# Optimization experiments

Hardware: AMD Instinct MI355X
Metric: run time of the kernel (lower is better)

The kernel has to match this reference:

```python
import jax, jax.numpy as jnp
import numpy as np

B, T, D, H = 4, 4096, 1024, 16
CAP = 0.5


def setup_inputs() -> dict:
    key = jax.random.key(0)
    ks = jax.random.split(key, 8)
    s = 0.02
    n = lambda k, shape: jax.random.normal(k, shape, dtype=jnp.float32) * s
    return {
        "x": jax.random.normal(ks[0], (B, T, D), dtype=jnp.float32),
        "w_router": n(ks[1], (D,)),
        "in_proj_w": n(ks[2], (3 * D, D)),
        "in_proj_b": jnp.zeros((3 * D,), jnp.float32),
        "out_proj_w": n(ks[3], (D, D)),
        "out_proj_b": jnp.zeros((D,), jnp.float32),
        "w1": n(ks[4], (4 * D, D)),
        "b1": jnp.zeros((4 * D,), jnp.float32),
        "w2": n(ks[5], (D, 4 * D)),
        "b2": jnp.zeros((D,), jnp.float32),
        "ln1_g": jnp.ones((D,), jnp.float32),
        "ln1_b": jnp.zeros((D,), jnp.float32),
        "ln2_g": jnp.ones((D,), jnp.float32),
        "ln2_b": jnp.zeros((D,), jnp.float32),
    }


def _ln(x, g, b, eps=1e-5):
    mu = jnp.mean(x, -1, keepdims=True)
    var = jnp.var(x, -1, keepdims=True)  # population variance, matches torch LayerNorm
    return (x - mu) * jax.lax.rsqrt(var + eps) * g + b


def reference(x, w_router, in_proj_w, in_proj_b, out_proj_w, out_proj_b,
              w1, b1, w2, b2, ln1_g, ln1_b, ln2_g, ln2_b):
    Bx, Tx, Dx = x.shape
    k = max(1, int(Tx * CAP))  # tokens routed through the block, same k for every batch row
    logits = x @ w_router  # (B,T) scalar router scores
    aux = jnp.mean(logits ** 2) * 0.01
    # top-k selection; sort indices ascending = boolean-mask gather order in torch
    idx = jnp.sort(jax.lax.top_k(logits, k)[1], axis=-1)  # (B,k)
    xs = jnp.take_along_axis(x, idx[:, :, None], axis=1)  # (B,k,D)

    h = _ln(xs, ln1_g, ln1_b)
    qkv = h @ in_proj_w.T + in_proj_b  # (B,k,3D)
    q, kk, v = jnp.split(qkv, 3, axis=-1)
    dh = Dx // H
    heads = lambda t: t.reshape(Bx, k, H, dh).transpose(0, 2, 1, 3)  # (B,H,k,dh)
    q, kk, v = heads(q), heads(kk), heads(v)
    scores = jnp.einsum('bhqd,bhkd->bhqk', q, kk) / jnp.sqrt(jnp.float32(dh))
    attn = jax.nn.softmax(scores, axis=-1)
    o = jnp.einsum('bhqk,bhkd->bhqd', attn, v).transpose(0, 2, 1, 3).reshape(Bx, k, Dx)
    o = o @ out_proj_w.T + out_proj_b
    xs = xs + o
    h2 = _ln(xs, ln2_g, ln2_b)
    ff = jax.nn.gelu(h2 @ w1.T + b1, approximate=False) @ w2.T + b2
    xs = xs + ff
    # scatter processed tokens back; unselected tokens pass through unchanged
    out = x.at[jnp.arange(Bx)[:, None], idx].set(xs)
    return out, aux
```

## Files before the change

### kernel.cpp

```cpp
#include <hip/hip_runtime.h>

#define B_    4
#define T_    4096
#define D_    1024
#define H_    16
#define DH_   64
#define KTOK  2048
#define MROWS (B_*KTOK)

typedef unsigned short u16;
typedef __attribute__((ext_vector_type(8))) short short8;
typedef __attribute__((ext_vector_type(4))) float f32x4;
typedef __attribute__((ext_vector_type(4))) unsigned int u32x4;
typedef __attribute__((ext_vector_type(2))) unsigned int u32x2;
typedef __attribute__((ext_vector_type(4))) unsigned short u16x4;

static __device__ __forceinline__ u16 f2bf(float f) {
  union { float f; unsigned int u; } a; a.f = f;
  unsigned int u = a.u;
  unsigned int r = (u + 0x7FFFu + ((u >> 16) & 1u)) >> 16;
  return (u16)r;
}

#if defined(__has_builtin)
#if __has_builtin(__builtin_amdgcn_exp2f)
#define EXP2F(x) __builtin_amdgcn_exp2f(x)
#endif
#endif
#ifndef EXP2F
#define EXP2F(x) exp2f(x)
#endif

static __device__ __forceinline__ unsigned int pkbf_t(float a, float b) {
  unsigned int ua = __builtin_bit_cast(unsigned int, a);
  unsigned int ub = __builtin_bit_cast(unsigned int, b);
  return __builtin_amdgcn_perm(ub, ua, 0x07060302u);
}

static __device__ __forceinline__ void gld_lds16(const u16* g, u16* l) {
  __builtin_amdgcn_global_load_lds((__attribute__((address_space(1))) void*)g,
                                   (__attribute__((address_space(3))) void*)l, 16, 0, 0);
}

__global__ void __launch_bounds__(256) router_kernel(const float* __restrict__ x,
    const float* __restrict__ wr, float* __restrict__ logits, float* __restrict__ auxacc)
{
  int tid = threadIdx.x; int lane = tid & 63, wave = tid >> 6;
  int row = blockIdx.x * 4 + wave;
  const float* xr = x + (size_t)row * D_;
  float dot = 0.f;
#pragma unroll
  for (int j = 0; j < 4; j++) {
    int c = j * 256 + lane * 4;
    f32x4 xv = *(const f32x4*)(xr + c);
    f32x4 wv = *(const f32x4*)(wr + c);
    dot += xv[0]*wv[0] + xv[1]*wv[1] + xv[2]*wv[2] + xv[3]*wv[3];
  }
#pragma unroll
  for (int d = 1; d < 64; d <<= 1) dot += __shfl_xor(dot, d);
  __shared__ float red[4];
  if (lane == 0) { logits[row] = dot; red[wave] = dot; }
  __syncthreads();
  if (tid == 0) {
    float a = red[0]*red[0] + red[1]*red[1] + red[2]*red[2] + red[3]*red[3];
    atomicAdd(auxacc, a);
  }
}

__global__ void __launch_bounds__(256) rank_kernel(const float* __restrict__ logits,
    int* __restrict__ mask, int* __restrict__ idx,
    const float* __restrict__ acc, float* __restrict__ auxout)
{
  __shared__ float ll[T_];
  int b = blockIdx.y;
  int tid = threadIdx.x;
  if (b == 0 && blockIdx.x == 0 && tid == 0)
    auxout[0] = acc[0] * (0.01f / (float)(B_ * T_));
  const float* lg = logits + (size_t)b * T_;
  for (int j = tid; j < T_; j += 256) ll[j] = lg[j];
  __syncthreads();
  int t = blockIdx.x * 256 + tid;
  float my = ll[t];
  int rank = 0;
  for (int j = 0; j < T_; j += 4) {
    f32x4 lj = *(const f32x4*)&ll[j];
    rank += (lj[0] > my) || (lj[0] == my && (j+0) < t);
    rank += (lj[1] > my) || (lj[1] == my && (j+1) < t);
    rank += (lj[2] > my) || (lj[2] == my && (j+2) < t);
    rank += (lj[3] > my) || (lj[3] == my && (j+3) < t);
  }
  int sel = (rank < KTOK) ? 1 : 0;
  mask[(size_t)b * T_ + t] = sel;
  if (sel) idx[b * KTOK + rank] = t;
}

__global__ void __launch_bounds__(256) passthru_kernel(const float* __restrict__ x,
    const int* __restrict__ mask, float* __restrict__ out)
{
  int row = blockIdx.x;
  if (mask[row]) return;
  const float* s = x + (size_t)row * D_;
  float* d = out + (size_t)row * D_;
  *(f32x4*)(d + threadIdx.x * 4) = *(const f32x4*)(s + threadIdx.x * 4);
}

template<bool GATHER>
__global__ void __launch_bounds__(256) ln_kernel(const float* __restrict__ src,
    const int* __restrict__ idx, const float* __restrict__ g, const float* __restrict__ bb,
    float* __restrict__ xs_out, u16* __restrict__ hout)
{
  int row = blockIdx.x;
  int tid = threadIdx.x;
  const float* srow;
  if (GATHER) {
    int b = row >> 11, i = row & (KTOK - 1);
    int t = idx[b * KTOK + i];
    srow = src + ((size_t)b * T_ + t) * D_;
  } else {
    srow = src + (size_t)row * D_;
  }
  f32x4 v = *(const f32x4*)(srow + tid * 4);
  float s  = v[0] + v[1] + v[2] + v[3];
  float sq = v[0]*v[0] + v[1]*v[1] + v[2]*v[2] + v[3]*v[3];
#pragma unroll
  for (int d = 1; d < 64; d <<= 1) { s += __shfl_xor(s, d); sq += __shfl_xor(sq, d); }
  __shared__ float rs[4], rq[4];
  int lane = tid & 63, wave = tid >> 6;
  if (lane == 0) { rs[wave] = s; rq[wave] = sq; }
  __syncthreads();
  s  = rs[0] + rs[1] + rs[2] + rs[3];
  sq = rq[0] + rq[1] + rq[2] + rq[3];
  float mean = s * (1.0f / D_);
  float var  = sq * (1.0f / D_) - mean * mean;
  float rstd = rsqrtf(var + 1e-5f);
  f32x4 gg = *(const f32x4*)(g + tid * 4);
  f32x4 bv = *(const f32x4*)(bb + tid * 4);
  if (GATHER) *(f32x4*)(xs_out + (size_t)row * D_ + tid * 4) = v;
  u16x4 o;
#pragma unroll
  for (int j = 0; j < 4; j++) o[j] = f2bf((v[j] - mean) * rstd * gg[j] + bv[j]);
  *(u16x4*)(hout + (size_t)row * D_ + tid * 4) = o;
}

__global__ void __launch_bounds__(256) f2bf_all(const float* __restrict__ s0, const float* __restrict__ s1,
    const float* __restrict__ s2, const float* __restrict__ s3,
    u16* __restrict__ d0, u16* __restrict__ d1, u16* __restrict__ d2, u16* __restrict__ d3)
{
  const size_t c0 = (size_t)3 * D_ * D_, c1 = (size_t)4 * D_ * D_, c2 = (size_t)8 * D_ * D_;
  size_t e = (size_t)blockIdx.x * 1024 + (size_t)threadIdx.x * 4;
  const float* s; u16* d; size_t off;
  if (e < c0)      { s = s0; d = d0; off = e; }
  else if (e < c1) { s = s1; d = d1; off = e - c0; }
  else if (e < c2) { s = s2; d = d2; off = e - c1; }
  else             { s = s3; d = d3; off = e - c2; }
  f32x4 v = *(const f32x4*)(s + off);
  u16x4 o; o[0]=f2bf(v[0]); o[1]=f2bf(v[1]); o[2]=f2bf(v[2]); o[3]=f2bf(v[3]);
  *(u16x4*)(d + off) = o;
}

template<int EPI>
__global__ void __launch_bounds__(256, 2) gemm_bt(
    const u16* __restrict__ A, const u16* __restrict__ W,
    const float* __restrict__ bias, float* __restrict__ xs,
    u16* __restrict__ Cb, float* __restrict__ outf,
    const int* __restrict__ idx, u16* __restrict__ vtb, int M, int N, int K)
{
  __shared__ u16 As[2][128 * 32];
  __shared__ u16 Ws[2][128 * 32];
  const int tid = threadIdx.x;
  const int lane = tid & 63, wave = tid >> 6;
  const int wm = wave >> 1, wn = wave & 1;
  const int m16 = lane & 15, quad = lane >> 4;

  const int gx = gridDim.x;
  const int id = blockIdx.y * gx + blockIdx.x;
  const int cpx = (gx * (int)gridDim.y) >> 3;
  const int tl = (id & 7) * cpx + (id >> 3);
  const int bx = tl % gx, by = tl / gx;

  const size_t arow0 = (size_t)by * 128;
  const size_t wrow0 = (size_t)bx * 128;
  const int r4 = lane >> 2, c8 = (lane & 3) * 8;

  const u16* ag0 = A + (arow0 + wave * 16 + r4) * (size_t)K + c8;
  const u16* ag1 = ag0 + (size_t)64 * K;
  const u16* wg0 = W + (wrow0 + wave * 16 + r4) * (size_t)K + c8;
  const u16* wg1 = wg0 + (size_t)64 * K;

  auto stage = [&](int k0, int s) {
    gld_lds16(ag0 + k0, &As[s][0] + (wave * 16) * 32);
    gld_lds16(ag1 + k0, &As[s][0] + (64 + wave * 16) * 32);
    gld_lds16(wg0 + k0, &Ws[s][0] + (wave * 16) * 32);
    gld_lds16(wg1 + k0, &Ws[s][0] + (64 + wave * 16) * 32);
  };

  f32x4 acc[4][4];
#pragma unroll
  for (int i = 0; i < 4; i++)
#pragma unroll
    for (int j = 0; j < 4; j++) acc[i][j] = (f32x4)0.0f;

  stage(0, 0);
  __syncthreads();
  int cur = 0;
  for (int k0 = 0; k0 < K; k0 += 32) {
    if (k0 + 32 < K) stage(k0 + 32, cur ^ 1);
    short8 af[4], wf[4];
#pragma unroll
    for (int mt = 0; mt < 4; mt++)
      af[mt] = *(const short8*)(&As[cur][0] + (wm * 64 + mt * 16 + m16) * 32 + quad * 8);
#pragma unroll
    for (int nt = 0; nt < 4; nt++)
      wf[nt] = *(const short8*)(&Ws[cur][0] + (wn * 64 + nt * 16 + m16) * 32 + quad * 8);
#pragma unroll
    for (int mt = 0; mt < 4; mt++)
#pragma unroll
      for (int nt = 0; nt < 4; nt++)
        acc[mt][nt] = __builtin_amdgcn_mfma_f32_16x16x32_bf16(af[mt], wf[nt], acc[mt][nt], 0, 0, 0);
    __syncthreads();
    cur ^= 1;
  }

#pragma unroll
  for (int mt = 0; mt < 4; mt++) {
#pragma unroll
    for (int nt = 0; nt < 4; nt++) {
      f32x4 a = acc[mt][nt];
      size_t col = wrow0 + wn * 64 + nt * 16 + m16;
      float bvv = bias[col];
      size_t rowb = arow0 + wm * 64 + mt * 16 + quad * 4;
      if (EPI == 0) {
        if ((int)col < 2 * D_) {
          float sc = ((int)col < D_) ? 0.18033688f : 1.0f;
#pragma unroll
          for (int r = 0; r < 4; r++)
            Cb[(rowb + r) * (size_t)N + col] = f2bf((a[r] + bvv) * sc);
        } else {
          int hdh = (int)col - 2 * D_;
          int bb  = (int)(rowb >> 11);
          int tok = (int)(rowb & (KTOK - 1));
          u16x4 o;
#pragma unroll
          for (int r = 0; r < 4; r++) o[r] = f2bf(a[r] + bvv);
          *(u16x4*)&vtb[(((size_t)(bb * H_) + (hdh >> 6)) * 64 + (hdh & 63)) * KTOK + tok] = o;
        }
      } else if (EPI == 1) {
#pragma unroll
        for (int r = 0; r < 4; r++) {
          size_t o = (rowb + r) * (size_t)N + col;
          xs[o] = xs[o] + (a[r] + bvv);
        }
      } else if (EPI == 2) {
#pragma unroll
        for (int r = 0; r < 4; r++) {
          float v = a[r] + bvv;
          float gv = 0.5f * v * (1.0f + erff(v * 0.70710678118654752f));
          Cb[(rowb + r) * (size_t)N + col] = f2bf(gv);
        }
      } else {
#pragma unroll
        for (int r = 0; r < 4; r++) {
          size_t row = rowb + r;
          int b = (int)(row >> 11);
          int i = (int)(row & (KTOK - 1));
          int t = idx[b * KTOK + i];
          float vv = xs[row * (size_t)D_ + col] + (a[r] + bvv);
          outf[((size_t)b * T_ + t) * D_ + col] = vv;
        }
      }
    }
  }
}

#define PSTR 72
__global__ void __launch_bounds__(256, 3) attn_kernel(const u16* __restrict__ qkv,
                                                      const u16* __restrict__ vtb,
                                                      u16* __restrict__ obuf)
{
  __shared__ u16 Ks[2][64 * 64];
  __shared__ u16 Vs[2][64 * 64];
  __shared__ u16 Ps[4][16 * PSTR];

  const int tid = threadIdx.x;
  const int lane = tid & 63, wave = tid >> 6;
  const int m16 = lane & 15, quad = lane >> 4;
  const int bh = blockIdx.x;
  const int b = bh >> 4, h = bh & 15;
  const int q0 = blockIdx.y * 128 + wave * 32;

  const u16* base = qkv + ((size_t)b * KTOK) * (3 * D_) + h * DH_;
  const u16* vb   = vtb + (size_t)bh * 64 * KTOK;

  short8 qf[2][2];
#pragma unroll
  for (int qh = 0; qh < 2; qh++) {
    const u16* qrow = base + (size_t)(q0 + qh * 16 + m16) * (3 * D_);
    qf[qh][0] = *(const short8*)(qrow + quad * 8);
    qf[qh][1] = *(const short8*)(qrow + 32 + quad * 8);
  }

  f32x4 oacc[2][4];
#pragma unroll
  for (int qh = 0; qh < 2; qh++)
#pragma unroll
    for (int nt = 0; nt < 4; nt++) oacc[qh][nt] = (f32x4)0.0f;
  f32x4 lsum[2] = {(f32x4)0.0f, (f32x4)0.0f};

  auto stage_tile = [&](const u16* g0, size_t rstride, u16* lds) {
#pragma unroll
    for (int c = 0; c < 2; c++) {
      int g = c * 256 + tid;
      int key = g >> 3;
      int cc = (g ^ key) & 7;
      gld_lds16(g0 + (size_t)key * rstride + cc * 8,
                lds + (size_t)(c * 256 + (tid & ~63)) * 8);
    }
  };

  stage_tile(base + D_, 3 * D_, &Ks[0][0]);
  stage_tile(vb, KTOK, &Vs[0][0]);
  __syncthreads();

  int buf = 0;
  for (int tk = 0; tk < KTOK; tk += 64) {
    if (tk + 64 < KTOK) {
      stage_tile(base + (size_t)(tk + 64) * (3 * D_) + D_, 3 * D_, &Ks[buf ^ 1][0]);
      stage_tile(vb + (tk + 64), KTOK, &Vs[buf ^ 1][0]);
    }
    const u16* Kb = &Ks[buf][0];
    const u16* Vb = &Vs[buf][0];

    f32x4 sacc[2][4];
#pragma unroll
    for (int qh = 0; qh < 2; qh++)
#pragma unroll
      for (int nt = 0; nt < 4; nt++) sacc[qh][nt] = (f32x4)0.0f;
    __builtin_amdgcn_s_setprio(1);
#pragma unroll
    for (int nt = 0; nt < 4; nt++) {
      int row = nt * 16 + m16;
      int sw = row & 7;
      short8 kf0 = *(const short8*)&Kb[row * 64 + ((quad ^ sw) * 8)];
      short8 kf1 = *(const short8*)&Kb[row * 64 + (((4 + quad) ^ sw) * 8)];
#pragma unroll
      for (int qh = 0; qh < 2; qh++) {
        sacc[qh][nt] = __builtin_amdgcn_mfma_f32_16x16x32_bf16(kf0, qf[qh][0], sacc[qh][nt], 0, 0, 0);
        sacc[qh][nt] = __builtin_amdgcn_mfma_f32_16x16x32_bf16(kf1, qf[qh][1], sacc[qh][nt], 0, 0, 0);
      }
    }
    __builtin_amdgcn_s_setprio(0);

    short8 vf[4][2];
#pragma unroll
    for (int nt = 0; nt < 4; nt++) {
      int row = nt * 16 + m16;
      int sw = row & 7;
      vf[nt][0] = *(const short8*)&Vb[row * 64 + ((quad ^ sw) * 8)];
      vf[nt][1] = *(const short8*)&Vb[row * 64 + (((4 + quad) ^ sw) * 8)];
    }

#pragma unroll
    for (int qh = 0; qh < 2; qh++) {
#pragma unroll
      for (int nt = 0; nt < 4; nt++) {
        f32x4 p;
#pragma unroll
        for (int r = 0; r < 4; r++) p[r] = EXP2F(sacc[qh][nt][r]);
        lsum[qh] += p;
        u32x2 w2; w2[0] = pkbf_t(p[0], p[1]); w2[1] = pkbf_t(p[2], p[3]);
        *(u32x2*)&Ps[wave][m16 * PSTR + nt * 16 + quad * 4] = w2;
      }
      short8 pa0 = *(const short8*)&Ps[wave][m16 * PSTR + quad * 8];
      short8 pa1 = *(const short8*)&Ps[wave][m16 * PSTR + 32 + quad * 8];
      __builtin_amdgcn_s_setprio(1);
#pragma unroll
      for (int nt = 0; nt < 4; nt++) {
        oacc[qh][nt] = __builtin_amdgcn_mfma_f32_16x16x32_bf16(pa0, vf[nt][0], oacc[qh][nt], 0, 0, 0);
        oacc[qh][nt] = __builtin_amdgcn_mfma_f32_16x16x32_bf16(pa1, vf[nt][1], oacc[qh][nt], 0, 0, 0);
      }
      __builtin_amdgcn_s_setprio(0);
    }

    __syncthreads();
    buf ^= 1;
  }

  float rl[2][4];
#pragma unroll
  for (int qh = 0; qh < 2; qh++) {
    float l = (lsum[qh][0] + lsum[qh][1]) + (lsum[qh][2] + lsum[qh][3]);
    l += __shfl_xor(l, 16);
    l += __shfl_xor(l, 32);
#pragma unroll
    for (int r = 0; r < 4; r++) {
      float lr = __shfl(l, (lane & 48) | (quad * 4 + r));
      rl[qh][r] = 1.0f / lr;
    }
  }

#pragma unroll
  for (int qh = 0; qh < 2; qh++)
#pragma unroll
    for (int nt = 0; nt < 4; nt++)
#pragma unroll
      for (int r = 0; r < 4; r++) {
        int qq = q0 + qh * 16 + quad * 4 + r;
        float v = oacc[qh][nt][r] * rl[qh][r];
        obuf[((size_t)b * KTOK + qq) * D_ + h * DH_ + nt * 16 + m16] = f2bf(v);
      }
}

extern "C" void kernel_launch(void* const* d_in, const int* in_sizes, int n_in,
                              void* d_out, int out_size, void* d_ws, size_t ws_size,
                              hipStream_t stream)
{
  (void)in_sizes; (void)n_in; (void)out_size; (void)ws_size;
  const float* x          = (const float*)d_in[0];
  const float* w_router   = (const float*)d_in[1];
  const float* in_proj_w  = (const float*)d_in[2];
  const float* in_proj_b  = (const float*)d_in[3];
  const float* out_proj_w = (const float*)d_in[4];
  const float* out_proj_b = (const float*)d_in[5];
  const float* w1         = (const float*)d_in[6];
  const float* b1         = (const float*)d_in[7];
  const float* w2         = (const float*)d_in[8];
  const float* b2         = (const float*)d_in[9];
  const float* ln1g       = (const float*)d_in[10];
  const float* ln1b       = (const float*)d_in[11];
  const float* ln2g       = (const float*)d_in[12];
  const float* ln2b       = (const float*)d_in[13];
  float* out = (float*)d_out;

  char* w = (char*)d_ws;
  auto alloc = [&](size_t bytes) -> char* {
    char* p = w; w += (bytes + 255) & ~(size_t)255; return p;
  };
  float* logits = (float*)alloc((size_t)B_ * T_ * 4);
  int*   mask   = (int*)  alloc((size_t)B_ * T_ * 4);
  int*   idx    = (int*)  alloc((size_t)B_ * KTOK * 4);
  float* auxacc = (float*)alloc(256);
  u16* inpw  = (u16*)alloc((size_t)3 * D_ * D_ * 2);
  u16* outpw = (u16*)alloc((size_t)D_ * D_ * 2);
  u16* w1b   = (u16*)alloc((size_t)4 * D_ * D_ * 2);
  u16* w2b   = (u16*)alloc((size_t)4 * D_ * D_ * 2);
  float* xs  = (float*)alloc((size_t)MROWS * D_ * 4);
  u16* hbuf  = (u16*)alloc((size_t)MROWS * D_ * 2);
  char* region = alloc((size_t)MROWS * 4 * D_ * 2);
  u16* qkvb = (u16*)region;
  u16* obuf = (u16*)(region + (size_t)MROWS * 3 * D_ * 2);
  u16* ffb  = (u16*)region;
  u16* vtb  = (u16*)alloc((size_t)B_ * H_ * DH_ * KTOK * 2);

  (void)hipMemsetAsync(auxacc, 0, 4, stream);

  router_kernel<<<B_ * T_ / 4, 256, 0, stream>>>(x, w_router, logits, auxacc);
  rank_kernel<<<dim3(T_ / 256, B_), 256, 0, stream>>>(logits, mask, idx, auxacc,
                                                      out + (size_t)B_ * T_ * D_);
  passthru_kernel<<<B_ * T_, 256, 0, stream>>>(x, mask, out);
  ln_kernel<true><<<MROWS, 256, 0, stream>>>(x, idx, ln1g, ln1b, xs, hbuf);

  f2bf_all<<<12 * D_ * D_ / 1024, 256, 0, stream>>>(in_proj_w, out_proj_w, w1, w2,
                                                    inpw, outpw, w1b, w2b);

  gemm_bt<0><<<dim3(3 * D_ / 128, MROWS / 128), 256, 0, stream>>>(
      hbuf, inpw, in_proj_b, nullptr, qkvb, nullptr, nullptr, vtb, MROWS, 3 * D_, D_);
  attn_kernel<<<dim3(B_ * H_, KTOK / 128), 256, 0, stream>>>(qkvb, vtb, obuf);
  gemm_bt<1><<<dim3(D_ / 128, MROWS / 128), 256, 0, stream>>>(
      obuf, outpw, out_proj_b, xs, nullptr, nullptr, nullptr, nullptr, MROWS, D_, D_);
  ln_kernel<false><<<MROWS, 256, 0, stream>>>(xs, nullptr, ln2g, ln2b, nullptr, hbuf);
  gemm_bt<2><<<dim3(4 * D_ / 128, MROWS / 128), 256, 0, stream>>>(
      hbuf, w1b, b1, nullptr, ffb, nullptr, nullptr, nullptr, MROWS, 4 * D_, D_);
  gemm_bt<3><<<dim3(D_ / 128, MROWS / 128), 256, 0, stream>>>(
      ffb, w2b, b2, xs, nullptr, out, idx, nullptr, MROWS, D_, 4 * D_);
}
```

Baseline: 747.2 us.

## Replace GEMM with 512-thread 256-wide tiled kernel and fuse passthrough into LN1

Swaps the 128x128 bf16 GEMM for a 512-thread kernel with 128x256 or 256x256 tiles. It uses BK=64 double-buffered, XOR-swizzled LDS, explicit vmcnt waits with raw barriers, and MFMA priority boosting to overlap loads with compute. The passthrough copy and the gathering LayerNorm are merged into one kernel. That kernel reads each row once and writes either to the output or to the compacted slot given by its rank. The larger tiles cut global traffic per FLOP, at the cost of more LDS and registers, fewer blocks on the D=1024 GEMMs, and fragile hand-written wait counts.

```diff
diff --git a/kernel.cpp b/kernel.cpp
--- a/kernel.cpp
+++ b/kernel.cpp
@@ -42,6 +42,8 @@
                                    (__attribute__((address_space(3))) void*)l, 16, 0, 0);
 }
 
+#define WAITV(N) asm volatile("s_waitcnt vmcnt(" #N ")" ::: "memory")
+
 __global__ void __launch_bounds__(256) router_kernel(const float* __restrict__ x,
     const float* __restrict__ wr, float* __restrict__ logits, float* __restrict__ auxacc)
 {
@@ -68,7 +70,7 @@
 }
 
 __global__ void __launch_bounds__(256) rank_kernel(const float* __restrict__ logits,
-    int* __restrict__ mask, int* __restrict__ idx,
+    int* __restrict__ rnk, int* __restrict__ idx,
     const float* __restrict__ acc, float* __restrict__ auxout)
 {
   __shared__ float ll[T_];
@@ -89,37 +91,24 @@
     rank += (lj[2] > my) || (lj[2] == my && (j+2) < t);
     rank += (lj[3] > my) || (lj[3] == my && (j+3) < t);
   }
-  int sel = (rank < KTOK) ? 1 : 0;
-  mask[(size_t)b * T_ + t] = sel;
-  if (sel) idx[b * KTOK + rank] = t;
-}
-
-__global__ void __launch_bounds__(256) passthru_kernel(const float* __restrict__ x,
-    const int* __restrict__ mask, float* __restrict__ out)
-{
-  int row = blockIdx.x;
-  if (mask[row]) return;
-  const float* s = x + (size_t)row * D_;
-  float* d = out + (size_t)row * D_;
-  *(f32x4*)(d + threadIdx.x * 4) = *(const f32x4*)(s + threadIdx.x * 4);
-}
-
-template<bool GATHER>
-__global__ void __launch_bounds__(256) ln_kernel(const float* __restrict__ src,
-    const int* __restrict__ idx, const float* __restrict__ g, const float* __restrict__ bb,
-    float* __restrict__ xs_out, u16* __restrict__ hout)
+  rnk[(size_t)b * T_ + t] = rank;
+  if (rank < KTOK) idx[b * KTOK + rank] = t;
+}
+
+__global__ void __launch_bounds__(256) lnpass_kernel(const float* __restrict__ x,
+    const int* __restrict__ rnk, const float* __restrict__ g, const float* __restrict__ bb,
+    float* __restrict__ xs_out, u16* __restrict__ hout, float* __restrict__ out)
 {
   int row = blockIdx.x;
   int tid = threadIdx.x;
-  const float* srow;
-  if (GATHER) {
-    int b = row >> 11, i = row & (KTOK - 1);
-    int t = idx[b * KTOK + i];
-    srow = src + ((size_t)b * T_ + t) * D_;
-  } else {
-    srow = src + (size_t)row * D_;
-  }
+  const float* srow = x + (size_t)row * D_;
   f32x4 v = *(const f32x4*)(srow + tid * 4);
+  int r = rnk[row];
+  if (r >= KTOK) {
+    *(f32x4*)(out + (size_t)row * D_ + tid * 4) = v;
+    return;
+  }
+  size_t mrow = (size_t)(row >> 12) * KTOK + r;
   float s  = v[0] + v[1] + v[2] + v[3];
   float sq = v[0]*v[0] + v[1]*v[1] + v[2]*v[2] + v[3]*v[3];
 #pragma unroll
@@ -135,7 +124,35 @@
   float rstd = rsqrtf(var + 1e-5f);
   f32x4 gg = *(const f32x4*)(g + tid * 4);
   f32x4 bv = *(const f32x4*)(bb + tid * 4);
-  if (GATHER) *(f32x4*)(xs_out + (size_t)row * D_ + tid * 4) = v;
+  *(f32x4*)(xs_out + mrow * D_ + tid * 4) = v;
+  u16x4 o;
+#pragma unroll
+  for (int j = 0; j < 4; j++) o[j] = f2bf((v[j] - mean) * rstd * gg[j] + bv[j]);
+  *(u16x4*)(hout + mrow * D_ + tid * 4) = o;
+}
+
+__global__ void __launch_bounds__(256) ln2_kernel(const float* __restrict__ src,
+    const float* __restrict__ g, const float* __restrict__ bb, u16* __restrict__ hout)
+{
+  int row = blockIdx.x;
+  int tid = threadIdx.x;
+  const float* srow = src + (size_t)row * D_;
+  f32x4 v = *(const f32x4*)(srow + tid * 4);
+  float s  = v[0] + v[1] + v[2] + v[3];
+  float sq = v[0]*v[0] + v[1]*v[1] + v[2]*v[2] + v[3]*v[3];
+#pragma unroll
+  for (int d = 1; d < 64; d <<= 1) { s += __shfl_xor(s, d); sq += __shfl_xor(sq, d); }
+  __shared__ float rs[4], rq[4];
+  int lane = tid & 63, wave = tid >> 6;
+  if (lane == 0) { rs[wave] = s; rq[wave] = sq; }
+  __syncthreads();
+  s  = rs[0] + rs[1] + rs[2] + rs[3];
+  sq = rq[0] + rq[1] + rq[2] + rq[3];
+  float mean = s * (1.0f / D_);
+  float var  = sq * (1.0f / D_) - mean * mean;
+  float rstd = rsqrtf(var + 1e-5f);
+  f32x4 gg = *(const f32x4*)(g + tid * 4);
+  f32x4 bv = *(const f32x4*)(bb + tid * 4);
   u16x4 o;
 #pragma unroll
   for (int j = 0; j < 4; j++) o[j] = f2bf((v[j] - mean) * rstd * gg[j] + bv[j]);
@@ -158,19 +175,22 @@
   *(u16x4*)(d + off) = o;
 }
 
-template<int EPI>
-__global__ void __launch_bounds__(256, 2) gemm_bt(
+template<int EPI, int HA>
+__global__ void __launch_bounds__(512, 2) gemm256(
     const u16* __restrict__ A, const u16* __restrict__ W,
     const float* __restrict__ bias, float* __restrict__ xs,
     u16* __restrict__ Cb, float* __restrict__ outf,
     const int* __restrict__ idx, u16* __restrict__ vtb, int M, int N, int K)
 {
-  __shared__ u16 As[2][128 * 32];
-  __shared__ u16 Ws[2][128 * 32];
+  __shared__ u16 Asm[2][HA][128 * 64];
+  __shared__ u16 Bsm[2][2][128 * 64];
+
   const int tid = threadIdx.x;
-  const int lane = tid & 63, wave = tid >> 6;
-  const int wm = wave >> 1, wn = wave & 1;
-  const int m16 = lane & 15, quad = lane >> 4;
+  const int lane = tid & 63;
+  const int w = tid >> 6;
+  const int m16 = lane & 15, quad = (lane >> 4) & 3;
+  const int rowA = (w >> 2) * 64;
+  const int rowB = (w & 3) * 32;
 
   const int gx = gridDim.x;
   const int id = blockIdx.y * gx + blockIdx.x;
@@ -178,94 +198,145 @@
   const int tl = (id & 7) * cpx + (id >> 3);
   const int bx = tl % gx, by = tl / gx;
 
-  const size_t arow0 = (size_t)by * 128;
-  const size_t wrow0 = (size_t)bx * 128;
-  const int r4 = lane >> 2, c8 = (lane & 3) * 8;
-
-  const u16* ag0 = A + (arow0 + wave * 16 + r4) * (size_t)K + c8;
-  const u16* ag1 = ag0 + (size_t)64 * K;
-  const u16* wg0 = W + (wrow0 + wave * 16 + r4) * (size_t)K + c8;
-  const u16* wg1 = wg0 + (size_t)64 * K;
-
-  auto stage = [&](int k0, int s) {
-    gld_lds16(ag0 + k0, &As[s][0] + (wave * 16) * 32);
-    gld_lds16(ag1 + k0, &As[s][0] + (64 + wave * 16) * 32);
-    gld_lds16(wg0 + k0, &Ws[s][0] + (wave * 16) * 32);
-    gld_lds16(wg1 + k0, &Ws[s][0] + (64 + wave * 16) * 32);
+  const int arow0 = by * (HA * 128);
+  const int wcol0 = bx * 256;
+
+  const int th8 = tid >> 3;
+  const int ccs = (tid ^ th8) & 7;
+  auto stage = [&](const u16* g0, u16* l0) {
+    gld_lds16(g0 + (size_t)th8 * K + ccs * 8,        l0 + (size_t)(tid & ~63) * 8);
+    gld_lds16(g0 + (size_t)(64 + th8) * K + ccs * 8, l0 + 4096 + (size_t)(tid & ~63) * 8);
   };
 
-  f32x4 acc[4][4];
-#pragma unroll
-  for (int i = 0; i < 4; i++)
-#pragma unroll
-    for (int j = 0; j < 4; j++) acc[i][j] = (f32x4)0.0f;
-
-  stage(0, 0);
-  __syncthreads();
-  int cur = 0;
-  for (int k0 = 0; k0 < K; k0 += 32) {
-    if (k0 + 32 < K) stage(k0 + 32, cur ^ 1);
-    short8 af[4], wf[4];
+  auto ldA = [&](short8 (&f)[4][2], const u16* h) {
+#pragma unroll
+    for (int mt = 0; mt < 4; mt++) {
+      int rr = rowA + mt * 16 + m16;
+      int sw = rr & 7;
+#pragma unroll
+      for (int kk = 0; kk < 2; kk++)
+        f[mt][kk] = *(const short8*)&h[rr * 64 + (((kk * 4 + quad) ^ sw) * 8)];
+    }
+  };
+  auto ldB = [&](short8 (&f)[2][2], const u16* h) {
+#pragma unroll
+    for (int nt = 0; nt < 2; nt++) {
+      int rb = rowB + nt * 16 + m16;
+      int sw = rb & 7;
+#pragma unroll
+      for (int kk = 0; kk < 2; kk++)
+        f[nt][kk] = *(const short8*)&h[rb * 64 + (((kk * 4 + quad) ^ sw) * 8)];
+    }
+  };
+
+  f32x4 acc[2 * HA][4][2];
+#pragma unroll
+  for (int q = 0; q < 2 * HA; q++)
 #pragma unroll
     for (int mt = 0; mt < 4; mt++)
-      af[mt] = *(const short8*)(&As[cur][0] + (wm * 64 + mt * 16 + m16) * 32 + quad * 8);
-#pragma unroll
-    for (int nt = 0; nt < 4; nt++)
-      wf[nt] = *(const short8*)(&Ws[cur][0] + (wn * 64 + nt * 16 + m16) * 32 + quad * 8);
-#pragma unroll
-    for (int mt = 0; mt < 4; mt++)
-#pragma unroll
-      for (int nt = 0; nt < 4; nt++)
-        acc[mt][nt] = __builtin_amdgcn_mfma_f32_16x16x32_bf16(af[mt], wf[nt], acc[mt][nt], 0, 0, 0);
-    __syncthreads();
-    cur ^= 1;
-  }
-
-#pragma unroll
-  for (int mt = 0; mt < 4; mt++) {
-#pragma unroll
-    for (int nt = 0; nt < 4; nt++) {
-      f32x4 a = acc[mt][nt];
-      size_t col = wrow0 + wn * 64 + nt * 16 + m16;
-      float bvv = bias[col];
-      size_t rowb = arow0 + wm * 64 + mt * 16 + quad * 4;
-      if (EPI == 0) {
-        if ((int)col < 2 * D_) {
-          float sc = ((int)col < D_) ? 0.18033688f : 1.0f;
-#pragma unroll
-          for (int r = 0; r < 4; r++)
-            Cb[(rowb + r) * (size_t)N + col] = f2bf((a[r] + bvv) * sc);
+#pragma unroll
+      for (int nt = 0; nt < 2; nt++) acc[q][mt][nt] = (f32x4)0.0f;
+
+#define MMQ(QD, FA, FB) do { \
+  __builtin_amdgcn_s_setprio(1); \
+  _Pragma("unroll") for (int mt = 0; mt < 4; mt++) \
+  _Pragma("unroll") for (int nt = 0; nt < 2; nt++) \
+  _Pragma("unroll") for (int kk = 0; kk < 2; kk++) \
+    acc[QD][mt][nt] = __builtin_amdgcn_mfma_f32_16x16x32_bf16(FA[mt][kk], FB[nt][kk], acc[QD][mt][nt], 0, 0, 0); \
+  __builtin_amdgcn_s_setprio(0); } while (0)
+
+  stage(A + (size_t)arow0 * K, &Asm[0][0][0]);
+  stage(W + (size_t)wcol0 * K, &Bsm[0][0][0]);
+  stage(W + (size_t)(wcol0 + 128) * K, &Bsm[0][1][0]);
+  if constexpr (HA == 2) stage(A + (size_t)(arow0 + 128) * K, &Asm[0][1][0]);
+
+  const int NT = K >> 6;
+  short8 af[4][2], af2[4][2], bf[2][2], bf2[2][2];
+
+  for (int t = 0; t < NT; t++) {
+    const int cur = t & 1, nxt = cur ^ 1;
+    const bool last = (t == NT - 1);
+    const int kn = (t + 1) * 64;
+
+    if constexpr (HA == 2) { WAITV(4); } else { WAITV(2); }
+    __builtin_amdgcn_s_barrier();
+    ldA(af, &Asm[cur][0][0]);
+    ldB(bf, &Bsm[cur][0][0]);
+    if (!last) stage(A + (size_t)arow0 * K + kn, &Asm[nxt][0][0]);
+    MMQ(0, af, bf);
+
+    if (!last) { if constexpr (HA == 2) { WAITV(4); } else { WAITV(2); } }
+    else       { if constexpr (HA == 2) { WAITV(2); } else { WAITV(0); } }
+    __builtin_amdgcn_s_barrier();
+    ldB(bf2, &Bsm[cur][1][0]);
+    if (!last) {
+      stage(W + (size_t)wcol0 * K + kn, &Bsm[nxt][0][0]);
+      if constexpr (HA == 1) stage(W + (size_t)(wcol0 + 128) * K + kn, &Bsm[nxt][1][0]);
+    }
+    MMQ(1, af, bf2);
+
+    if constexpr (HA == 2) {
+      if (!last) { WAITV(4); } else { WAITV(0); }
+      __builtin_amdgcn_s_barrier();
+      ldA(af2, &Asm[cur][1][0]);
+      if (!last) stage(W + (size_t)(wcol0 + 128) * K + kn, &Bsm[nxt][1][0]);
+      MMQ(2, af2, bf);
+      if (!last) stage(A + (size_t)(arow0 + 128) * K + kn, &Asm[nxt][1][0]);
+      MMQ(3, af2, bf2);
+    }
+  }
+#undef MMQ
+
+#pragma unroll
+  for (int qd = 0; qd < 2 * HA; qd++) {
+    const int ha = (HA == 2) ? (qd >> 1) : 0;
+    const int hb = (HA == 2) ? (qd & 1) : qd;
+#pragma unroll
+    for (int mt = 0; mt < 4; mt++) {
+#pragma unroll
+      for (int nt = 0; nt < 2; nt++) {
+        f32x4 a = acc[qd][mt][nt];
+        size_t col = (size_t)wcol0 + hb * 128 + (w & 3) * 32 + nt * 16 + m16;
+        float bvv = bias[col];
+        size_t rowb = (size_t)arow0 + ha * 128 + (w >> 2) * 64 + mt * 16 + quad * 4;
+        if (EPI == 0) {
+          if ((int)col < 2 * D_) {
+            float sc = ((int)col < D_) ? 0.18033688f : 1.0f;
+#pragma unroll
+            for (int r = 0; r < 4; r++)
+              Cb[(rowb + r) * (size_t)N + col] = f2bf((a[r] + bvv) * sc);
+          } else {
+            int hdh = (int)col - 2 * D_;
+            int bb2 = (int)(rowb >> 11);
+            int tok = (int)(rowb & (KTOK - 1));
+            u16x4 o;
+#pragma unroll
+            for (int r = 0; r < 4; r++) o[r] = f2bf(a[r] + bvv);
+            *(u16x4*)&vtb[(((size_t)(bb2 * H_) + (hdh >> 6)) * 64 + (hdh & 63)) * KTOK + tok] = o;
+          }
+        } else if (EPI == 1) {
+#pragma unroll
+          for (int r = 0; r < 4; r++) {
+            size_t o = (rowb + r) * (size_t)N + col;
+            xs[o] = xs[o] + (a[r] + bvv);
+          }
+        } else if (EPI == 2) {
+#pragma unroll
+          for (int r = 0; r < 4; r++) {
+            float v = a[r] + bvv;
+            float gv = 0.5f * v * (1.0f + erff(v * 0.70710678118654752f));
+            Cb[(rowb + r) * (size_t)N + col] = f2bf(gv);
+          }
         } else {
-          int hdh = (int)col - 2 * D_;
-          int bb  = (int)(rowb >> 11);
-          int tok = (int)(rowb & (KTOK - 1));
-          u16x4 o;
-#pragma unroll
-          for (int r = 0; r < 4; r++) o[r] = f2bf(a[r] + bvv);
-          *(u16x4*)&vtb[(((size_t)(bb * H_) + (hdh >> 6)) * 64 + (hdh & 63)) * KTOK + tok] = o;
-        }
-      } else if (EPI == 1) {
-#pragma unroll
-        for (int r = 0; r < 4; r++) {
-          size_t o = (rowb + r) * (size_t)N + col;
-          xs[o] = xs[o] + (a[r] + bvv);
-        }
-      } else if (EPI == 2) {
-#pragma unroll
-        for (int r = 0; r < 4; r++) {
-          float v = a[r] + bvv;
-          float gv = 0.5f * v * (1.0f + erff(v * 0.70710678118654752f));
-          Cb[(rowb + r) * (size_t)N + col] = f2bf(gv);
-        }
-      } else {
-#pragma unroll
-        for (int r = 0; r < 4; r++) {
-          size_t row = rowb + r;
-          int b = (int)(row >> 11);
-          int i = (int)(row & (KTOK - 1));
-          int t = idx[b * KTOK + i];
-          float vv = xs[row * (size_t)D_ + col] + (a[r] + bvv);
-          outf[((size_t)b * T_ + t) * D_ + col] = vv;
+#pragma unroll
+          for (int r = 0; r < 4; r++) {
+            size_t row = rowb + r;
+            int b = (int)(row >> 11);
+            int i = (int)(row & (KTOK - 1));
+            int t = idx[b * KTOK + i];
+            float vv = xs[row * (size_t)D_ + col] + (a[r] + bvv);
+            outf[((size_t)b * T_ + t) * D_ + col] = vv;
+          }
         }
       }
     }
@@ -436,7 +507,7 @@
     char* p = w; w += (bytes + 255) & ~(size_t)255; return p;
   };
   float* logits = (float*)alloc((size_t)B_ * T_ * 4);
-  int*   mask   = (int*)  alloc((size_t)B_ * T_ * 4);
+  int*   rnk    = (int*)  alloc((size_t)B_ * T_ * 4);
   int*   idx    = (int*)  alloc((size_t)B_ * KTOK * 4);
   float* auxacc = (float*)alloc(256);
   u16* inpw  = (u16*)alloc((size_t)3 * D_ * D_ * 2);
@@ -454,22 +525,21 @@
   (void)hipMemsetAsync(auxacc, 0, 4, stream);
 
   router_kernel<<<B_ * T_ / 4, 256, 0, stream>>>(x, w_router, logits, auxacc);
-  rank_kernel<<<dim3(T_ / 256, B_), 256, 0, stream>>>(logits, mask, idx, auxacc,
+  rank_kernel<<<dim3(T_ / 256, B_), 256, 0, stream>>>(logits, rnk, idx, auxacc,
                                                       out + (size_t)B_ * T_ * D_);
-  passthru_kernel<<<B_ * T_, 256, 0, stream>>>(x, mask, out);
-  ln_kernel<true><<<MROWS, 256, 0, stream>>>(x, idx, ln1g, ln1b, xs, hbuf);
+  lnpass_kernel<<<B_ * T_, 256, 0, stream>>>(x, rnk, ln1g, ln1b, xs, hbuf, out);
 
   f2bf_all<<<12 * D_ * D_ / 1024, 256, 0, stream>>>(in_proj_w, out_proj_w, w1, w2,
                                                     inpw, outpw, w1b, w2b);
 
-  gemm_bt<0><<<dim3(3 * D_ / 128, MROWS / 128), 256, 0, stream>>>(
+  gemm256<0, 1><<<dim3(3 * D_ / 256, MROWS / 128), 512, 0, stream>>>(
       hbuf, inpw, in_proj_b, nullptr, qkvb, nullptr, nullptr, vtb, MROWS, 3 * D_, D_);
   attn_kernel<<<dim3(B_ * H_, KTOK / 128), 256, 0, stream>>>(qkvb, vtb, obuf);
-  gemm_bt<1><<<dim3(D_ / 128, MROWS / 128), 256, 0, stream>>>(
+  gemm256<1, 1><<<dim3(D_ / 256, MROWS / 128), 512, 0, stream>>>(
       obuf, outpw, out_proj_b, xs, nullptr, nullptr, nullptr, nullptr, MROWS, D_, D_);
-  ln_kernel<false><<<MROWS, 256, 0, stream>>>(xs, nullptr, ln2g, ln2b, nullptr, hbuf);
-  gemm_bt<2><<<dim3(4 * D_ / 128, MROWS / 128), 256, 0, stream>>>(
+  ln2_kernel<<<MROWS, 256, 0, stream>>>(xs, ln2g, ln2b, hbuf);
+  gemm256<2, 2><<<dim3(4 * D_ / 256, MROWS / 256), 512, 0, stream>>>(
       hbuf, w1b, b1, nullptr, ffb, nullptr, nullptr, nullptr, MROWS, 4 * D_, D_);
-  gemm_bt<3><<<dim3(D_ / 128, MROWS / 128), 256, 0, stream>>>(
+  gemm256<3, 1><<<dim3(D_ / 256, MROWS / 128), 512, 0, stream>>>(
       ffb, w2b, b2, xs, nullptr, out, idx, nullptr, MROWS, D_, 4 * D_);
 }
```

Result: slower. 801.8 us (+7.3%).
